# Optimization experiments

Hardware: AMD Instinct MI355X
Metric: run time of the kernel (lower is better)

## Reference

```python
import jax, jax.numpy as jnp
import numpy as np

DIM = 1024
DEPTH = 8
DIM_HEAD = 64
HEADS = 16
NUM_Q = 16
EMB = 768
OUT = 1024
FF_INNER = 4 * DIM
INNER = DIM_HEAD * HEADS  # 1024
B, N1 = 64, 577
EPS = 1e-5


def _ln(x, g, b):
    mu = jnp.mean(x, axis=-1, keepdims=True)
    var = jnp.mean((x - mu) ** 2, axis=-1, keepdims=True)
    return (x - mu) * jax.lax.rsqrt(var + EPS) * g + b


def setup_inputs() -> dict:
    key = jax.random.key(0)
    ks = jax.random.split(key, 16)
    std = 0.02
    inp = {
        'x': jax.random.normal(ks[0], (B, N1, EMB), jnp.float32),
        'queries': jax.random.normal(ks[1], (1, NUM_Q, DIM), jnp.float32) / DIM ** 0.5,
        'proj_in_w': jax.random.normal(ks[2], (EMB, DIM), jnp.float32) * std,
        'proj_in_b': jnp.zeros((DIM,), jnp.float32),
        'ln1_g': jnp.ones((DEPTH, DIM), jnp.float32),
        'ln1_b': jnp.zeros((DEPTH, DIM), jnp.float32),
        'ln2_g': jnp.ones((DEPTH, DIM), jnp.float32),
        'ln2_b': jnp.zeros((DEPTH, DIM), jnp.float32),
        'wq': jax.random.normal(ks[3], (DEPTH, DIM, INNER), jnp.float32) * std,
        'wkv': jax.random.normal(ks[4], (DEPTH, DIM, 2 * INNER), jnp.float32) * std,
        'wo': jax.random.normal(ks[5], (DEPTH, INNER, DIM), jnp.float32) * std,
        'ffln_g': jnp.ones((DEPTH, DIM), jnp.float32),
        'ffln_b': jnp.zeros((DEPTH, DIM), jnp.float32),
        'w1': jax.random.normal(ks[6], (DEPTH, DIM, FF_INNER), jnp.float32) * std,
        'w2': jax.random.normal(ks[7], (DEPTH, FF_INNER, DIM), jnp.float32) * std,
        'proj_out_w': jax.random.normal(ks[8], (DIM, OUT), jnp.float32) * std,
        'proj_out_b': jnp.zeros((OUT,), jnp.float32),
        'nout_g': jnp.ones((OUT,), jnp.float32),
        'nout_b': jnp.zeros((OUT,), jnp.float32),
    }
    return inp


def reference(x, queries, proj_in_w, proj_in_b, ln1_g, ln1_b, ln2_g, ln2_b,
              wq, wkv, wo, ffln_g, ffln_b, w1, w2,
              proj_out_w, proj_out_b, nout_g, nout_b):
    b = x.shape[0]
    xp = x @ proj_in_w + proj_in_b          # (b, n1, dim)
    latents0 = jnp.broadcast_to(queries, (b, NUM_Q, DIM))
    scale = DIM_HEAD ** -0.25               # applied to both q and k

    def layer(latents, p):
        (g1, b1, g2, b2, Wq, Wkv, Wo, gf, bf, W1, W2) = p
        xn = _ln(xp, g1, b1)                # (b, n1, dim)
        lt = _ln(latents, g2, b2)           # (b, nq, dim)
        q = lt @ Wq                         # (b, nq, inner)
        kv_in = jnp.concatenate([xn, lt], axis=1)   # (b, n1+nq, dim)
        kv = kv_in @ Wkv                    # (b, n1+nq, 2*inner)
        k, v = jnp.split(kv, 2, axis=-1)
        L = kv_in.shape[1]
        qh = q.reshape(b, NUM_Q, HEADS, DIM_HEAD).transpose(0, 2, 1, 3)
        kh = k.reshape(b, L, HEADS, DIM_HEAD).transpose(0, 2, 1, 3)
        vh = v.reshape(b, L, HEADS, DIM_HEAD).transpose(0, 2, 1, 3)
        logits = jnp.einsum('bhqd,bhkd->bhqk', qh * scale, kh * scale)
        w = jax.nn.softmax(logits.astype(jnp.float32), axis=-1).astype(logits.dtype)
        o = jnp.einsum('bhqk,bhkd->bhqd', w, vh)
        o = o.transpose(0, 2, 1, 3).reshape(b, NUM_Q, INNER) @ Wo
        latents = o + latents
        h = _ln(latents, gf, bf) @ W1
        h = jax.nn.gelu(h, approximate=False)
        latents = h @ W2 + latents
        return latents, None

    params = (ln1_g, ln1_b, ln2_g, ln2_b, wq, wkv, wo, ffln_g, ffln_b, w1, w2)
    latents, _ = jax.lax.scan(layer, latents0, params)
    out = latents @ proj_out_w + proj_out_b
    return _ln(out, nout_g, nout_b)
```

## Files before the change

### kernel.cpp

```cpp
#include <hip/hip_runtime.h>
#include <hip/hip_bf16.h>
#include <math.h>

#define DEV __device__ __forceinline__

typedef __bf16 bf16x8 __attribute__((ext_vector_type(8)));
typedef float f32x4 __attribute__((ext_vector_type(4)));
typedef unsigned short u16x8 __attribute__((ext_vector_type(8)));
typedef unsigned short u16x4 __attribute__((ext_vector_type(4)));

DEV float b2f(unsigned short u){ unsigned int i = ((unsigned int)u)<<16; float f; __builtin_memcpy(&f,&i,4); return f; }
DEV unsigned short f2b(float x){ unsigned int i; __builtin_memcpy(&i,&x,4); unsigned int r = i + 0x7FFFu + ((i>>16)&1u); return (unsigned short)(r>>16); }

DEV int swz(int row, int elem){ return row*64 + ((((elem>>3) ^ row) & 7)<<3) + (elem&7); }

enum { EPI_F32=0, EPI_GELU=2, EPI_RESF32=3 };

template<int BM, int BN>
__global__ __launch_bounds__(256)
void gemm2(const unsigned short* __restrict__ A, const unsigned short* __restrict__ Bt,
           const float* __restrict__ bias, unsigned short* __restrict__ Out,
           int M, int N, int K, int NT)
{
    constexpr int MR = BM/32, NR = BN/32;
    constexpr int LA = BM/32, LB = BN/32;
    __shared__ unsigned short As[2][BM*64];
    __shared__ unsigned short Bs[2][BN*64];
    const int tid  = threadIdx.x;
    const int lane = tid & 63;
    const int wave = tid >> 6;
    const int wr = wave >> 1, wc = wave & 1;
    const int chunk = gridDim.x >> 3;
    const int nb = (blockIdx.x & 7)*chunk + (blockIdx.x >> 3);
    const int nt = nb % NT, mt = nb / NT;
    const int lr = lane >> 3;
    const int lc = lane & 7;

    f32x4 acc[MR][NR];
    #pragma unroll
    for (int m=0;m<MR;m++)
      #pragma unroll
      for (int n=0;n<NR;n++) acc[m][n] = f32x4{0.f,0.f,0.f,0.f};

    const unsigned short* pA[LA];
    const unsigned short* pB[LB];
    #pragma unroll
    for (int i=0;i<LA;i++){
      int s = wave*LA + i; int row = s*8 + lr;
      int gr = mt*BM + row; if (gr > M-1) gr = M-1;
      pA[i] = A + (size_t)gr*K + (((lc ^ row)&7)<<3);
    }
    #pragma unroll
    for (int i=0;i<LB;i++){
      int s = wave*LB + i; int row = s*8 + lr;
      pB[i] = Bt + (size_t)(nt*BN+row)*K + (((lc ^ row)&7)<<3);
    }

    auto stage = [&](int buf, int k0){
      #pragma unroll
      for (int i=0;i<LA;i++){
        int s = wave*LA + i;
        __builtin_amdgcn_global_load_lds((const unsigned int*)(pA[i]+k0), (unsigned int*)&As[buf][s*512], 16, 0, 0);
      }
      #pragma unroll
      for (int i=0;i<LB;i++){
        int s = wave*LB + i;
        __builtin_amdgcn_global_load_lds((const unsigned int*)(pB[i]+k0), (unsigned int*)&Bs[buf][s*512], 16, 0, 0);
      }
    };

    stage(0, 0);
    const int nk = K / 64;
    #pragma unroll 1
    for (int kt=0; kt<nk; kt++){
      const int cur = kt & 1;
      asm volatile("s_waitcnt vmcnt(0)" ::: "memory");
      __builtin_amdgcn_s_barrier();
      __builtin_amdgcn_sched_barrier(0);
      if (kt+1 < nk) stage(cur^1, (kt+1)*64);
      #pragma unroll
      for (int kk=0; kk<2; kk++){
        bf16x8 av[MR], bv[NR];
        #pragma unroll
        for (int m=0;m<MR;m++){
          int r = wr*(BM/2) + m*16 + (lane&15);
          av[m] = (bf16x8)(*reinterpret_cast<const u16x8*>(&As[cur][swz(r, kk*32 + (lane>>4)*8)]));
        }
        #pragma unroll
        for (int n=0;n<NR;n++){
          int r = wc*(BN/2) + n*16 + (lane&15);
          bv[n] = (bf16x8)(*reinterpret_cast<const u16x8*>(&Bs[cur][swz(r, kk*32 + (lane>>4)*8)]));
        }
        #pragma unroll
        for (int m=0;m<MR;m++)
          #pragma unroll
          for (int n=0;n<NR;n++)
            acc[m][n] = __builtin_amdgcn_mfma_f32_16x16x32_bf16(av[m], bv[n], acc[m][n], 0, 0, 0);
      }
    }

    #pragma unroll
    for (int m=0;m<MR;m++){
      #pragma unroll
      for (int n=0;n<NR;n++){
        #pragma unroll
        for (int r=0;r<4;r++){
          int row = mt*BM + wr*(BM/2) + m*16 + (lane>>4)*4 + r;
          int col = nt*BN + wc*(BN/2) + n*16 + (lane&15);
          if (row < M){
            float v = acc[m][n][r];
            if (bias) v += bias[col];
            Out[(size_t)row*N + col] = f2b(v);
          }
        }
      }
    }
}

template<int EPI>
__global__ __launch_bounds__(256)
void gemm_sp2(const unsigned short* __restrict__ AH, const unsigned short* __restrict__ AL,
              const unsigned short* __restrict__ BH, const unsigned short* __restrict__ BL,
              const float* __restrict__ bias, const float* __restrict__ Res,
              void* __restrict__ Out, unsigned short* __restrict__ OutL,
              int M, int N, int K, int NT)
{
    constexpr int MR=2, NR=2;
    __shared__ unsigned short As[2][2][64*64];
    __shared__ unsigned short Bs[2][2][64*64];
    const int tid  = threadIdx.x;
    const int lane = tid & 63;
    const int wave = tid >> 6;
    const int wr = wave >> 1, wc = wave & 1;
    const int chunk = gridDim.x >> 3;
    const int nb = (blockIdx.x & 7)*chunk + (blockIdx.x >> 3);
    const int nt = nb % NT, mt = nb / NT;
    const int lr = lane >> 3;
    const int lc = lane & 7;

    f32x4 acc[MR][NR];
    #pragma unroll
    for (int m=0;m<MR;m++)
      #pragma unroll
      for (int n=0;n<NR;n++) acc[m][n] = f32x4{0.f,0.f,0.f,0.f};

    const unsigned short *pAH[2], *pAL[2], *pBH[2], *pBL[2];
    #pragma unroll
    for (int i=0;i<2;i++){
      int s = wave*2 + i; int row = s*8 + lr; int scol = ((lc ^ row)&7)<<3;
      size_t aofs = (size_t)(mt*64+row)*K + scol;
      size_t bofs = (size_t)(nt*64+row)*K + scol;
      pAH[i] = AH + aofs; pAL[i] = AL + aofs;
      pBH[i] = BH + bofs; pBL[i] = BL + bofs;
    }

    auto stage = [&](int buf, int k0){
      #pragma unroll
      for (int i=0;i<2;i++){
        int s = wave*2 + i;
        __builtin_amdgcn_global_load_lds((const unsigned int*)(pAH[i]+k0), (unsigned int*)&As[buf][0][s*512], 16, 0, 0);
        __builtin_amdgcn_global_load_lds((const unsigned int*)(pAL[i]+k0), (unsigned int*)&As[buf][1][s*512], 16, 0, 0);
        __builtin_amdgcn_global_load_lds((const unsigned int*)(pBH[i]+k0), (unsigned int*)&Bs[buf][0][s*512], 16, 0, 0);
        __builtin_amdgcn_global_load_lds((const unsigned int*)(pBL[i]+k0), (unsigned int*)&Bs[buf][1][s*512], 16, 0, 0);
      }
    };

    stage(0, 0);
    const int nk = K / 64;
    #pragma unroll 1
    for (int kt=0; kt<nk; kt++){
      const int cur = kt & 1;
      asm volatile("s_waitcnt vmcnt(0)" ::: "memory");
      __builtin_amdgcn_s_barrier();
      __builtin_amdgcn_sched_barrier(0);
      if (kt+1 < nk) stage(cur^1, (kt+1)*64);
      #pragma unroll
      for (int kk=0; kk<2; kk++){
        bf16x8 ah[MR], al[MR], bh[NR], bl[NR];
        #pragma unroll
        for (int m=0;m<MR;m++){
          int a = swz(wr*32 + m*16 + (lane&15), kk*32 + (lane>>4)*8);
          ah[m] = (bf16x8)(*reinterpret_cast<const u16x8*>(&As[cur][0][a]));
          al[m] = (bf16x8)(*reinterpret_cast<const u16x8*>(&As[cur][1][a]));
        }
        #pragma unroll
        for (int n=0;n<NR;n++){
          int a = swz(wc*32 + n*16 + (lane&15), kk*32 + (lane>>4)*8);
          bh[n] = (bf16x8)(*reinterpret_cast<const u16x8*>(&Bs[cur][0][a]));
          bl[n] = (bf16x8)(*reinterpret_cast<const u16x8*>(&Bs[cur][1][a]));
        }
        #pragma unroll
        for (int m=0;m<MR;m++)
          #pragma unroll
          for (int n=0;n<NR;n++){
            acc[m][n] = __builtin_amdgcn_mfma_f32_16x16x32_bf16(ah[m], bh[n], acc[m][n], 0, 0, 0);
            acc[m][n] = __builtin_amdgcn_mfma_f32_16x16x32_bf16(ah[m], bl[n], acc[m][n], 0, 0, 0);
            acc[m][n] = __builtin_amdgcn_mfma_f32_16x16x32_bf16(al[m], bh[n], acc[m][n], 0, 0, 0);
          }
      }
    }

    #pragma unroll
    for (int m=0;m<MR;m++){
      #pragma unroll
      for (int n=0;n<NR;n++){
        #pragma unroll
        for (int r=0;r<4;r++){
          int row = mt*64 + wr*32 + m*16 + (lane>>4)*4 + r;
          int col = nt*64 + wc*32 + n*16 + (lane&15);
          float v = acc[m][n][r];
          if (bias) v += bias[col];
          if constexpr (EPI==EPI_GELU){
            v = 0.5f*v*(1.0f + erff(v*0.70710678118654752f));
            unsigned short hi = f2b(v);
            ((unsigned short*)Out)[(size_t)row*N + col] = hi;
            OutL[(size_t)row*N + col] = f2b(v - b2f(hi));
          } else {
            if constexpr (EPI==EPI_RESF32) v += Res[(size_t)row*N + col];
            ((float*)Out)[(size_t)row*N + col] = v;
          }
        }
      }
    }
}

enum { OM_F32=0, OM_BF16=1, OM_SPLIT=2 };
template<bool INF32, int OM, bool HASGB>
__global__ __launch_bounds__(256)
void ln_rows(const void* __restrict__ In, void* __restrict__ Out,
             unsigned short* __restrict__ OutL,
             const float* __restrict__ g, const float* __restrict__ bb)
{
  const int row = blockIdx.x;
  const int tid = threadIdx.x;
  const size_t base = (size_t)row*1024 + tid*4;
  float v[4];
  if constexpr (INF32){
    f32x4 t = *reinterpret_cast<const f32x4*>((const float*)In + base);
    v[0]=t[0]; v[1]=t[1]; v[2]=t[2]; v[3]=t[3];
  } else {
    u16x4 t = *reinterpret_cast<const u16x4*>((const unsigned short*)In + base);
    #pragma unroll
    for (int j=0;j<4;j++) v[j] = b2f(t[j]);
  }
  float s = v[0]+v[1]+v[2]+v[3];
  float q = v[0]*v[0]+v[1]*v[1]+v[2]*v[2]+v[3]*v[3];
  #pragma unroll
  for (int o=32;o>0;o>>=1){ s += __shfl_xor(s,o,64); q += __shfl_xor(q,o,64); }
  __shared__ float sm[8];
  const int wave = tid>>6, lane = tid&63;
  if (lane==0){ sm[wave] = s; sm[4+wave] = q; }
  __syncthreads();
  s = sm[0]+sm[1]+sm[2]+sm[3];
  q = sm[4]+sm[5]+sm[6]+sm[7];
  const float mean = s*(1.f/1024.f);
  const float rstd = rsqrtf(fmaxf(q*(1.f/1024.f) - mean*mean, 0.f) + 1e-5f);
  #pragma unroll
  for (int j=0;j<4;j++){
    float t2 = (v[j]-mean)*rstd;
    if constexpr (HASGB) t2 = t2*g[tid*4+j] + bb[tid*4+j];
    v[j] = t2;
  }
  if constexpr (OM==OM_F32){
    f32x4 t{v[0],v[1],v[2],v[3]};
    *reinterpret_cast<f32x4*>((float*)Out + base) = t;
  } else if constexpr (OM==OM_BF16){
    u16x4 t{f2b(v[0]),f2b(v[1]),f2b(v[2]),f2b(v[3])};
    *reinterpret_cast<u16x4*>((unsigned short*)Out + base) = t;
  } else {
    u16x4 h{f2b(v[0]),f2b(v[1]),f2b(v[2]),f2b(v[3])};
    u16x4 l{f2b(v[0]-b2f(h[0])),f2b(v[1]-b2f(h[1])),f2b(v[2]-b2f(h[2])),f2b(v[3]-b2f(h[3]))};
    *reinterpret_cast<u16x4*>((unsigned short*)Out + base) = h;
    *reinterpret_cast<u16x4*>(OutL + base) = l;
  }
}

template<bool LO>
__global__ __launch_bounds__(256)
void transpose_cvt_b(const float* __restrict__ W, const float* __restrict__ rs,
                     unsigned short* __restrict__ Wt, unsigned short* __restrict__ Wtlo,
                     int K, int N, size_t wLS, size_t tLS, int dstRowOff)
{
  const int l = blockIdx.z;
  const float* Wl = W + (size_t)l*wLS;
  __shared__ float t[32][33];
  const int tx = threadIdx.x & 31, ty = threadIdx.x >> 5;
  const int n0 = blockIdx.x*32, k0 = blockIdx.y*32;
  #pragma unroll
  for (int j=0;j<4;j++){
    int r = ty + j*8;
    float w = Wl[(size_t)(k0+r)*N + n0 + tx];
    if (rs) w *= rs[l*1024 + k0+r];
    t[r][tx] = w;
  }
  __syncthreads();
  #pragma unroll
  for (int j=0;j<4;j++){
    int r = ty + j*8;
    float w = t[tx][r];
    unsigned short hi = f2b(w);
    size_t di = (size_t)l*tLS + (size_t)(dstRowOff + n0 + r)*K + k0 + tx;
    Wt[di] = hi;
    if constexpr (LO) Wtlo[di] = f2b(w - b2f(hi));
  }
}

__global__ __launch_bounds__(256)
void biaskv_kernel(const float* __restrict__ ln1b, const float* __restrict__ wkv,
                   float* __restrict__ out)
{
  const int l = blockIdx.y;
  const int n = blockIdx.x*256 + threadIdx.x;
  const float* b1 = ln1b + l*1024;
  const float* W  = wkv + (size_t)l*1024*2048;
  float s = 0.f;
  for (int k=0;k<1024;k++) s += b1[k]*W[(size_t)k*2048 + n];
  out[l*2048 + n] = s;
}

__global__ __launch_bounds__(256)
void init_latents(const float* __restrict__ Q, float* __restrict__ L)
{
  size_t idx = ((size_t)blockIdx.x*256 + threadIdx.x)*4;
  int row = (int)(idx >> 10);
  int col = (int)(idx & 1023);
  f32x4 t = *reinterpret_cast<const f32x4*>(Q + (size_t)(row & 15)*1024 + col);
  *reinterpret_cast<f32x4*>(L + idx) = t;
}

__global__ __launch_bounds__(256)
void cvt_f32_bf16(const float* __restrict__ In, unsigned short* __restrict__ Out, size_t n4)
{
  size_t i = (size_t)blockIdx.x*256 + threadIdx.x;
  if (i >= n4) return;
  f32x4 t = *reinterpret_cast<const f32x4*>(In + i*4);
  u16x4 u{f2b(t[0]),f2b(t[1]),f2b(t[2]),f2b(t[3])};
  *reinterpret_cast<u16x4*>(Out + i*4) = u;
}

__global__ __launch_bounds__(256)
void cvt_f32b_pair(const float* __restrict__ In, unsigned short* __restrict__ Oh,
                   unsigned short* __restrict__ Ol)
{
  size_t idx = ((size_t)blockIdx.x*256 + threadIdx.x)*4;
  f32x4 t = *reinterpret_cast<const f32x4*>(In + idx);
  u16x4 h{f2b(t[0]),f2b(t[1]),f2b(t[2]),f2b(t[3])};
  u16x4 l{f2b(t[0]-b2f(h[0])),f2b(t[1]-b2f(h[1])),f2b(t[2]-b2f(h[2])),f2b(t[3]-b2f(h[3]))};
  *reinterpret_cast<u16x4*>(Oh + idx) = h;
  *reinterpret_cast<u16x4*>(Ol + idx) = l;
}

__global__ __launch_bounds__(256)
void attn_kernel(const float* __restrict__ QKVf,
                 const unsigned short* __restrict__ KVX,
                 unsigned short* __restrict__ ATTOh,
                 unsigned short* __restrict__ ATTOl)
{
  __shared__ float qs[16][64];
  __shared__ float ws[16][600];
  const int tid = threadIdx.x;
  const int bh = blockIdx.x;
  const int b = bh >> 4, h = bh & 15;

  {
    int idx = tid*4;
    int qi = idx >> 6, d = idx & 63;
    f32x4 t = *reinterpret_cast<const f32x4*>(QKVf + (size_t)(b*16+qi)*3072 + h*64 + d);
    #pragma unroll
    for (int j=0;j<4;j++) qs[qi][d+j] = 0.125f * t[j];
  }
  __syncthreads();

  for (int r = tid; r < 593; r += 256){
    float a[16];
    #pragma unroll
    for (int qi=0;qi<16;qi++) a[qi] = 0.f;
    if (r < 577){
      const unsigned short* krow = KVX + ((size_t)(b*577 + r)*2048 + h*64);
      #pragma unroll 4
      for (int d4=0; d4<16; d4++){
        u16x4 k4 = *reinterpret_cast<const u16x4*>(krow + d4*4);
        float kf0=b2f(k4[0]), kf1=b2f(k4[1]), kf2=b2f(k4[2]), kf3=b2f(k4[3]);
        #pragma unroll
        for (int qi=0;qi<16;qi++){
          f32x4 q4 = *reinterpret_cast<const f32x4*>(&qs[qi][d4*4]);
          a[qi] += q4[0]*kf0 + q4[1]*kf1 + q4[2]*kf2 + q4[3]*kf3;
        }
      }
    } else {
      const float* krow = QKVf + (size_t)(b*16 + (r-577))*3072 + 1024 + h*64;
      #pragma unroll 4
      for (int d4=0; d4<16; d4++){
        f32x4 k4 = *reinterpret_cast<const f32x4*>(krow + d4*4);
        #pragma unroll
        for (int qi=0;qi<16;qi++){
          f32x4 q4 = *reinterpret_cast<const f32x4*>(&qs[qi][d4*4]);
          a[qi] += q4[0]*k4[0] + q4[1]*k4[1] + q4[2]*k4[2] + q4[3]*k4[3];
        }
      }
    }
    #pragma unroll
    for (int qi=0;qi<16;qi++) ws[qi][r] = a[qi];
  }
  __syncthreads();

  const int wave = tid>>6, lane = tid&63;
  for (int qi = wave; qi < 16; qi += 4){
    float m = -1e30f;
    for (int r = lane; r < 593; r += 64) m = fmaxf(m, ws[qi][r]);
    #pragma unroll
    for (int o=32;o>0;o>>=1) m = fmaxf(m, __shfl_xor(m,o,64));
    float s = 0.f;
    for (int r = lane; r < 593; r += 64){ float e = expf(ws[qi][r]-m); ws[qi][r] = e; s += e; }
    #pragma unroll
    for (int o=32;o>0;o>>=1) s += __shfl_xor(s,o,64);
    float inv = 1.f/s;
    for (int r = lane; r < 593; r += 64) ws[qi][r] *= inv;
  }
  __syncthreads();

  const int d = tid & 63, qg = tid >> 6;
  float o0=0.f,o1=0.f,o2=0.f,o3=0.f;
  for (int rr=0; rr<576; rr+=4){
    f32x4 w0 = *reinterpret_cast<const f32x4*>(&ws[qg   ][rr]);
    f32x4 w1 = *reinterpret_cast<const f32x4*>(&ws[qg+4 ][rr]);
    f32x4 w2 = *reinterpret_cast<const f32x4*>(&ws[qg+8 ][rr]);
    f32x4 w3 = *reinterpret_cast<const f32x4*>(&ws[qg+12][rr]);
    #pragma unroll
    for (int j=0;j<4;j++){
      const unsigned short* vrow = KVX + ((size_t)(b*577 + rr + j)*2048 + 1024 + h*64);
      float v = b2f(vrow[d]);
      o0 += w0[j]*v; o1 += w1[j]*v; o2 += w2[j]*v; o3 += w3[j]*v;
    }
  }
  {
    float v = b2f(KVX[(size_t)(b*577 + 576)*2048 + 1024 + h*64 + d]);
    o0 += ws[qg][576]*v; o1 += ws[qg+4][576]*v; o2 += ws[qg+8][576]*v; o3 += ws[qg+12][576]*v;
  }
  for (int r=577; r<593; r++){
    float v = QKVf[(size_t)(b*16 + (r-577))*3072 + 2048 + h*64 + d];
    o0 += ws[qg][r]*v; o1 += ws[qg+4][r]*v; o2 += ws[qg+8][r]*v; o3 += ws[qg+12][r]*v;
  }
  float ov[4] = {o0,o1,o2,o3};
  #pragma unroll
  for (int j=0;j<4;j++){
    size_t idx = (size_t)(b*16+qg+4*j)*1024 + h*64 + d;
    unsigned short hi = f2b(ov[j]);
    ATTOh[idx] = hi;
    ATTOl[idx] = f2b(ov[j] - b2f(hi));
  }
}

extern "C" void kernel_launch(void* const* d_in, const int* in_sizes, int n_in,
                              void* d_out, int out_size, void* d_ws, size_t ws_size,
                              hipStream_t stream)
{
  const float* x    = (const float*)d_in[0];
  const float* qry  = (const float*)d_in[1];
  const float* piw  = (const float*)d_in[2];
  const float* pib  = (const float*)d_in[3];
  const float* ln1g = (const float*)d_in[4];
  const float* ln1b = (const float*)d_in[5];
  const float* ln2g = (const float*)d_in[6];
  const float* ln2b = (const float*)d_in[7];
  const float* wq   = (const float*)d_in[8];
  const float* wkv  = (const float*)d_in[9];
  const float* wo   = (const float*)d_in[10];
  const float* ffg  = (const float*)d_in[11];
  const float* ffb  = (const float*)d_in[12];
  const float* w1   = (const float*)d_in[13];
  const float* w2   = (const float*)d_in[14];
  const float* pow_ = (const float*)d_in[15];
  const float* pob  = (const float*)d_in[16];
  const float* ng   = (const float*)d_in[17];
  const float* nb   = (const float*)d_in[18];

  const int MROWS = 64*577;
  char* wsb = (char*)d_ws;
  size_t off = 0;
  auto alloc = [&](size_t bytes)->char*{
    char* p = wsb + off; off = (off + bytes + 255) & ~(size_t)255; return p;
  };
  unsigned short* XB     = (unsigned short*)alloc((size_t)36992*768*2);
  unsigned short* XP     = (unsigned short*)alloc((size_t)36992*1024*2);
  unsigned short* KVX    = (unsigned short*)alloc((size_t)36992*2048*2);
  unsigned short* WpiT   = (unsigned short*)alloc((size_t)1024*768*2);
  unsigned short* WkvTs  = (unsigned short*)alloc((size_t)8*2048*1024*2);
  unsigned short* WqkvT  = (unsigned short*)alloc((size_t)8*3072*1024*2);
  unsigned short* WqkvTl = (unsigned short*)alloc((size_t)8*3072*1024*2);
  unsigned short* WoT    = (unsigned short*)alloc((size_t)8*1024*1024*2);
  unsigned short* WoTl   = (unsigned short*)alloc((size_t)8*1024*1024*2);
  unsigned short* W1T    = (unsigned short*)alloc((size_t)4096*1024*2);
  unsigned short* W1Tl   = (unsigned short*)alloc((size_t)4096*1024*2);
  unsigned short* W2T    = (unsigned short*)alloc((size_t)1024*4096*2);
  unsigned short* W2Tl   = (unsigned short*)alloc((size_t)1024*4096*2);
  float*          BKV    = (float*)alloc((size_t)8*2048*4);
  unsigned short* LTh    = (unsigned short*)alloc((size_t)1024*1024*2);
  unsigned short* LTl    = (unsigned short*)alloc((size_t)1024*1024*2);
  float*          QKVf   = (float*)alloc((size_t)1024*3072*4);
  unsigned short* ATTOh  = (unsigned short*)alloc((size_t)1024*1024*2);
  unsigned short* ATTOl  = (unsigned short*)alloc((size_t)1024*1024*2);
  unsigned short* FFHh   = (unsigned short*)alloc((size_t)1024*4096*2);
  unsigned short* FFHl   = (unsigned short*)alloc((size_t)1024*4096*2);
  unsigned short* LATBh  = (unsigned short*)alloc((size_t)1024*1024*2);
  unsigned short* LATBl  = (unsigned short*)alloc((size_t)1024*1024*2);
  float*          LATF   = (float*)alloc((size_t)1024*1024*4);
  if (off > ws_size) return;

  dim3 blk(256);

  cvt_f32_bf16<<<dim3((36928*768/4 + 255)/256), blk, 0, stream>>>(x, XB, (size_t)36928*768/4);
  transpose_cvt_b<false><<<dim3(32,24,1), blk, 0, stream>>>(piw, nullptr, WpiT, nullptr, 768, 1024, 0, 0, 0);
  transpose_cvt_b<false><<<dim3(64,32,8), blk, 0, stream>>>(wkv, ln1g, WkvTs, nullptr, 1024, 2048, (size_t)1024*2048, (size_t)2048*1024, 0);
  transpose_cvt_b<true ><<<dim3(32,32,8), blk, 0, stream>>>(wq,  nullptr, WqkvT, WqkvTl, 1024, 1024, (size_t)1024*1024, (size_t)3072*1024, 0);
  transpose_cvt_b<true ><<<dim3(64,32,8), blk, 0, stream>>>(wkv, nullptr, WqkvT, WqkvTl, 1024, 2048, (size_t)1024*2048, (size_t)3072*1024, 1024);
  transpose_cvt_b<true ><<<dim3(32,32,8), blk, 0, stream>>>(wo,  nullptr, WoT, WoTl, 1024, 1024, (size_t)1024*1024, (size_t)1024*1024, 0);
  biaskv_kernel<<<dim3(8,8), blk, 0, stream>>>(ln1b, wkv, BKV);
  init_latents<<<dim3(1024), blk, 0, stream>>>(qry, LATF);

  gemm2<128,128><<<dim3(8*289), blk, 0, stream>>>(XB, WpiT, pib, XP, MROWS, 1024, 768, 8);
  ln_rows<false,OM_BF16,false><<<dim3(MROWS), blk, 0, stream>>>(XP, XP, nullptr, nullptr, nullptr);

  for (int l=0; l<8; l++){
    transpose_cvt_b<true><<<dim3(128,32,1), blk, 0, stream>>>(w1 + (size_t)l*1024*4096, nullptr, W1T, W1Tl, 1024, 4096, 0, 0, 0);
    transpose_cvt_b<true><<<dim3(32,128,1), blk, 0, stream>>>(w2 + (size_t)l*4096*1024, nullptr, W2T, W2Tl, 4096, 1024, 0, 0, 0);

    ln_rows<true,OM_SPLIT,true><<<dim3(1024), blk, 0, stream>>>(LATF, LTh, LTl, ln2g + l*1024, ln2b + l*1024);
    gemm_sp2<EPI_F32><<<dim3(16*48), blk, 0, stream>>>(
        LTh, LTl, WqkvT + (size_t)l*3072*1024, WqkvTl + (size_t)l*3072*1024,
        nullptr, nullptr, QKVf, nullptr, 1024, 3072, 1024, 48);
    gemm2<128,128><<<dim3(16*289), blk, 0, stream>>>(
        XP, WkvTs + (size_t)l*2048*1024, BKV + l*2048, KVX, MROWS, 2048, 1024, 16);
    attn_kernel<<<dim3(1024), blk, 0, stream>>>(QKVf, KVX, ATTOh, ATTOl);
    gemm_sp2<EPI_RESF32><<<dim3(16*16), blk, 0, stream>>>(
        ATTOh, ATTOl, WoT + (size_t)l*1024*1024, WoTl + (size_t)l*1024*1024,
        nullptr, LATF, LATF, nullptr, 1024, 1024, 1024, 16);
    ln_rows<true,OM_SPLIT,true><<<dim3(1024), blk, 0, stream>>>(LATF, LTh, LTl, ffg + l*1024, ffb + l*1024);
    gemm_sp2<EPI_GELU><<<dim3(16*64), blk, 0, stream>>>(
        LTh, LTl, W1T, W1Tl, nullptr, nullptr, FFHh, FFHl, 1024, 4096, 1024, 64);
    gemm_sp2<EPI_RESF32><<<dim3(16*16), blk, 0, stream>>>(
        FFHh, FFHl, W2T, W2Tl, nullptr, LATF, LATF, nullptr, 1024, 1024, 4096, 16);
  }

  transpose_cvt_b<true><<<dim3(32,32,1), blk, 0, stream>>>(pow_, nullptr, W1T, W1Tl, 1024, 1024, 0, 0, 0);
  cvt_f32b_pair<<<dim3(1024), blk, 0, stream>>>(LATF, LATBh, LATBl);
  gemm_sp2<EPI_F32><<<dim3(16*16), blk, 0, stream>>>(
      LATBh, LATBl, W1T, W1Tl, pob, nullptr, QKVf, nullptr, 1024, 1024, 1024, 16);
  ln_rows<true,OM_F32,true><<<dim3(1024), blk, 0, stream>>>(QKVf, d_out, nullptr, ng, nb);
}
```

Baseline: 5.926 ms.

## Replace LDS double-buffer DMA with register-staged two-deep prefetch in GEMMs

Both GEMM kernels drop the direct global-to-LDS loads and the double-buffered shared tiles. They now prefetch two k-tiles into registers, then commit each into a single shared tile between barriers before computing on it. This halves shared memory per block, which may raise occupancy, and keeps two global loads in flight. The cost is more VGPRs, extra LDS write instructions and four barriers per two k-steps. The loop assumes K/64 is even.

```diff
diff --git a/kernel.cpp b/kernel.cpp
--- a/kernel.cpp
+++ b/kernel.cpp
@@ -24,8 +24,8 @@
 {
     constexpr int MR = BM/32, NR = BN/32;
     constexpr int LA = BM/32, LB = BN/32;
-    __shared__ unsigned short As[2][BM*64];
-    __shared__ unsigned short Bs[2][BN*64];
+    __shared__ unsigned short As[BM*64];
+    __shared__ unsigned short Bs[BN*64];
     const int tid  = threadIdx.x;
     const int lane = tid & 63;
     const int wave = tid >> 6;
@@ -33,8 +33,6 @@
     const int chunk = gridDim.x >> 3;
     const int nb = (blockIdx.x & 7)*chunk + (blockIdx.x >> 3);
     const int nt = nb % NT, mt = nb / NT;
-    const int lr = lane >> 3;
-    const int lc = lane & 7;
 
     f32x4 acc[MR][NR];
     #pragma unroll
@@ -42,54 +40,60 @@
       #pragma unroll
       for (int n=0;n<NR;n++) acc[m][n] = f32x4{0.f,0.f,0.f,0.f};
 
-    const unsigned short* pA[LA];
-    const unsigned short* pB[LB];
+    const unsigned short* pA[LA]; const unsigned short* pB[LB];
+    int dA[LA], dB[LB];
     #pragma unroll
     for (int i=0;i<LA;i++){
-      int s = wave*LA + i; int row = s*8 + lr;
+      int e = (i*256+tid)*8; int row = e>>6, col = e&63;
       int gr = mt*BM + row; if (gr > M-1) gr = M-1;
-      pA[i] = A + (size_t)gr*K + (((lc ^ row)&7)<<3);
+      pA[i] = A + (size_t)gr*K + col;
+      dA[i] = swz(row,col);
     }
     #pragma unroll
     for (int i=0;i<LB;i++){
-      int s = wave*LB + i; int row = s*8 + lr;
-      pB[i] = Bt + (size_t)(nt*BN+row)*K + (((lc ^ row)&7)<<3);
-    }
-
-    auto stage = [&](int buf, int k0){
-      #pragma unroll
-      for (int i=0;i<LA;i++){
-        int s = wave*LA + i;
-        __builtin_amdgcn_global_load_lds((const unsigned int*)(pA[i]+k0), (unsigned int*)&As[buf][s*512], 16, 0, 0);
-      }
-      #pragma unroll
-      for (int i=0;i<LB;i++){
-        int s = wave*LB + i;
-        __builtin_amdgcn_global_load_lds((const unsigned int*)(pB[i]+k0), (unsigned int*)&Bs[buf][s*512], 16, 0, 0);
-      }
-    };
-
-    stage(0, 0);
-    const int nk = K / 64;
-    #pragma unroll 1
-    for (int kt=0; kt<nk; kt++){
-      const int cur = kt & 1;
-      asm volatile("s_waitcnt vmcnt(0)" ::: "memory");
-      __builtin_amdgcn_s_barrier();
-      __builtin_amdgcn_sched_barrier(0);
-      if (kt+1 < nk) stage(cur^1, (kt+1)*64);
+      int e = (i*256+tid)*8; int row = e>>6, col = e&63;
+      pB[i] = Bt + (size_t)(nt*BN+row)*K + col;
+      dB[i] = swz(row,col);
+    }
+
+    u16x8 rA0[LA], rB0[LB], rA1[LA], rB1[LB];
+    auto issue0 = [&](int k0){
+      #pragma unroll
+      for (int i=0;i<LA;i++) rA0[i] = *reinterpret_cast<const u16x8*>(pA[i]+k0);
+      #pragma unroll
+      for (int i=0;i<LB;i++) rB0[i] = *reinterpret_cast<const u16x8*>(pB[i]+k0);
+    };
+    auto issue1 = [&](int k0){
+      #pragma unroll
+      for (int i=0;i<LA;i++) rA1[i] = *reinterpret_cast<const u16x8*>(pA[i]+k0);
+      #pragma unroll
+      for (int i=0;i<LB;i++) rB1[i] = *reinterpret_cast<const u16x8*>(pB[i]+k0);
+    };
+    auto commit0 = [&](){
+      #pragma unroll
+      for (int i=0;i<LA;i++) *reinterpret_cast<u16x8*>(&As[dA[i]]) = rA0[i];
+      #pragma unroll
+      for (int i=0;i<LB;i++) *reinterpret_cast<u16x8*>(&Bs[dB[i]]) = rB0[i];
+    };
+    auto commit1 = [&](){
+      #pragma unroll
+      for (int i=0;i<LA;i++) *reinterpret_cast<u16x8*>(&As[dA[i]]) = rA1[i];
+      #pragma unroll
+      for (int i=0;i<LB;i++) *reinterpret_cast<u16x8*>(&Bs[dB[i]]) = rB1[i];
+    };
+    auto compute = [&](){
       #pragma unroll
       for (int kk=0; kk<2; kk++){
         bf16x8 av[MR], bv[NR];
         #pragma unroll
         for (int m=0;m<MR;m++){
           int r = wr*(BM/2) + m*16 + (lane&15);
-          av[m] = (bf16x8)(*reinterpret_cast<const u16x8*>(&As[cur][swz(r, kk*32 + (lane>>4)*8)]));
+          av[m] = (bf16x8)(*reinterpret_cast<const u16x8*>(&As[swz(r, kk*32 + (lane>>4)*8)]));
         }
         #pragma unroll
         for (int n=0;n<NR;n++){
           int r = wc*(BN/2) + n*16 + (lane&15);
-          bv[n] = (bf16x8)(*reinterpret_cast<const u16x8*>(&Bs[cur][swz(r, kk*32 + (lane>>4)*8)]));
+          bv[n] = (bf16x8)(*reinterpret_cast<const u16x8*>(&Bs[swz(r, kk*32 + (lane>>4)*8)]));
         }
         #pragma unroll
         for (int m=0;m<MR;m++)
@@ -97,6 +101,22 @@
           for (int n=0;n<NR;n++)
             acc[m][n] = __builtin_amdgcn_mfma_f32_16x16x32_bf16(av[m], bv[n], acc[m][n], 0, 0, 0);
       }
+    };
+
+    const int nk = K / 64;
+    issue0(0); issue1(64);
+    #pragma unroll 1
+    for (int kt=0; kt<nk; kt+=2){
+      __syncthreads();
+      commit0();
+      __syncthreads();
+      if (kt+2 < nk) issue0((kt+2)*64);
+      compute();
+      __syncthreads();
+      commit1();
+      __syncthreads();
+      if (kt+3 < nk) issue1((kt+3)*64);
+      compute();
     }
 
     #pragma unroll
@@ -126,8 +146,8 @@
               int M, int N, int K, int NT)
 {
     constexpr int MR=2, NR=2;
-    __shared__ unsigned short As[2][2][64*64];
-    __shared__ unsigned short Bs[2][2][64*64];
+    __shared__ unsigned short As[2*64*64];
+    __shared__ unsigned short Bs[2*64*64];
     const int tid  = threadIdx.x;
     const int lane = tid & 63;
     const int wave = tid >> 6;
@@ -135,8 +155,6 @@
     const int chunk = gridDim.x >> 3;
     const int nb = (blockIdx.x & 7)*chunk + (blockIdx.x >> 3);
     const int nt = nb % NT, mt = nb / NT;
-    const int lr = lane >> 3;
-    const int lc = lane & 7;
 
     f32x4 acc[MR][NR];
     #pragma unroll
@@ -144,50 +162,71 @@
       #pragma unroll
       for (int n=0;n<NR;n++) acc[m][n] = f32x4{0.f,0.f,0.f,0.f};
 
-    const unsigned short *pAH[2], *pAL[2], *pBH[2], *pBL[2];
+    const unsigned short *pA[2], *pB[2];
+    int dst[2];
     #pragma unroll
     for (int i=0;i<2;i++){
-      int s = wave*2 + i; int row = s*8 + lr; int scol = ((lc ^ row)&7)<<3;
-      size_t aofs = (size_t)(mt*64+row)*K + scol;
-      size_t bofs = (size_t)(nt*64+row)*K + scol;
-      pAH[i] = AH + aofs; pAL[i] = AL + aofs;
-      pBH[i] = BH + bofs; pBL[i] = BL + bofs;
-    }
-
-    auto stage = [&](int buf, int k0){
+      int e = (i*256+tid)*8; int row = e>>6, col = e&63;
+      pA[i] = AH + (size_t)(mt*64+row)*K + col;
+      pB[i] = BH + (size_t)(nt*64+row)*K + col;
+      dst[i] = swz(row,col);
+    }
+    const size_t dAL = (size_t)(AL - AH);
+    const size_t dBL = (size_t)(BL - BH);
+
+    u16x8 rAH0[2], rAL0[2], rBH0[2], rBL0[2];
+    u16x8 rAH1[2], rAL1[2], rBH1[2], rBL1[2];
+    auto issue0 = [&](int k0){
       #pragma unroll
       for (int i=0;i<2;i++){
-        int s = wave*2 + i;
-        __builtin_amdgcn_global_load_lds((const unsigned int*)(pAH[i]+k0), (unsigned int*)&As[buf][0][s*512], 16, 0, 0);
-        __builtin_amdgcn_global_load_lds((const unsigned int*)(pAL[i]+k0), (unsigned int*)&As[buf][1][s*512], 16, 0, 0);
-        __builtin_amdgcn_global_load_lds((const unsigned int*)(pBH[i]+k0), (unsigned int*)&Bs[buf][0][s*512], 16, 0, 0);
-        __builtin_amdgcn_global_load_lds((const unsigned int*)(pBL[i]+k0), (unsigned int*)&Bs[buf][1][s*512], 16, 0, 0);
-      }
-    };
-
-    stage(0, 0);
-    const int nk = K / 64;
-    #pragma unroll 1
-    for (int kt=0; kt<nk; kt++){
-      const int cur = kt & 1;
-      asm volatile("s_waitcnt vmcnt(0)" ::: "memory");
-      __builtin_amdgcn_s_barrier();
-      __builtin_amdgcn_sched_barrier(0);
-      if (kt+1 < nk) stage(cur^1, (kt+1)*64);
+        rAH0[i] = *reinterpret_cast<const u16x8*>(pA[i]+k0);
+        rAL0[i] = *reinterpret_cast<const u16x8*>(pA[i]+dAL+k0);
+        rBH0[i] = *reinterpret_cast<const u16x8*>(pB[i]+k0);
+        rBL0[i] = *reinterpret_cast<const u16x8*>(pB[i]+dBL+k0);
+      }
+    };
+    auto issue1 = [&](int k0){
+      #pragma unroll
+      for (int i=0;i<2;i++){
+        rAH1[i] = *reinterpret_cast<const u16x8*>(pA[i]+k0);
+        rAL1[i] = *reinterpret_cast<const u16x8*>(pA[i]+dAL+k0);
+        rBH1[i] = *reinterpret_cast<const u16x8*>(pB[i]+k0);
+        rBL1[i] = *reinterpret_cast<const u16x8*>(pB[i]+dBL+k0);
+      }
+    };
+    auto commit0 = [&](){
+      #pragma unroll
+      for (int i=0;i<2;i++){
+        *reinterpret_cast<u16x8*>(&As[dst[i]])      = rAH0[i];
+        *reinterpret_cast<u16x8*>(&As[4096+dst[i]]) = rAL0[i];
+        *reinterpret_cast<u16x8*>(&Bs[dst[i]])      = rBH0[i];
+        *reinterpret_cast<u16x8*>(&Bs[4096+dst[i]]) = rBL0[i];
+      }
+    };
+    auto commit1 = [&](){
+      #pragma unroll
+      for (int i=0;i<2;i++){
+        *reinterpret_cast<u16x8*>(&As[dst[i]])      = rAH1[i];
+        *reinterpret_cast<u16x8*>(&As[4096+dst[i]]) = rAL1[i];
+        *reinterpret_cast<u16x8*>(&Bs[dst[i]])      = rBH1[i];
+        *reinterpret_cast<u16x8*>(&Bs[4096+dst[i]]) = rBL1[i];
+      }
+    };
+    auto compute = [&](){
       #pragma unroll
       for (int kk=0; kk<2; kk++){
         bf16x8 ah[MR], al[MR], bh[NR], bl[NR];
         #pragma unroll
         for (int m=0;m<MR;m++){
           int a = swz(wr*32 + m*16 + (lane&15), kk*32 + (lane>>4)*8);
-          ah[m] = (bf16x8)(*reinterpret_cast<const u16x8*>(&As[cur][0][a]));
-          al[m] = (bf16x8)(*reinterpret_cast<const u16x8*>(&As[cur][1][a]));
+          ah[m] = (bf16x8)(*reinterpret_cast<const u16x8*>(&As[a]));
+          al[m] = (bf16x8)(*reinterpret_cast<const u16x8*>(&As[4096 + a]));
         }
         #pragma unroll
         for (int n=0;n<NR;n++){
           int a = swz(wc*32 + n*16 + (lane&15), kk*32 + (lane>>4)*8);
-          bh[n] = (bf16x8)(*reinterpret_cast<const u16x8*>(&Bs[cur][0][a]));
-          bl[n] = (bf16x8)(*reinterpret_cast<const u16x8*>(&Bs[cur][1][a]));
+          bh[n] = (bf16x8)(*reinterpret_cast<const u16x8*>(&Bs[a]));
+          bl[n] = (bf16x8)(*reinterpret_cast<const u16x8*>(&Bs[4096 + a]));
         }
         #pragma unroll
         for (int m=0;m<MR;m++)
@@ -198,6 +237,22 @@
             acc[m][n] = __builtin_amdgcn_mfma_f32_16x16x32_bf16(al[m], bh[n], acc[m][n], 0, 0, 0);
           }
       }
+    };
+
+    const int nk = K / 64;
+    issue0(0); issue1(64);
+    #pragma unroll 1
+    for (int kt=0; kt<nk; kt+=2){
+      __syncthreads();
+      commit0();
+      __syncthreads();
+      if (kt+2 < nk) issue0((kt+2)*64);
+      compute();
+      __syncthreads();
+      commit1();
+      __syncthreads();
+      if (kt+3 < nk) issue1((kt+3)*64);
+      compute();
     }
 
     #pragma unroll
```

Result: faster. 5.335 ms (-10.0%).
